# Kernel tuning notes

Measured on AMD Instinct MI355X. Metric: run time of the kernel, lower is better.

The kernel has to match this reference:

```python
import jax, jax.numpy as jnp
import numpy as np

jax.config.update("jax_enable_x64", True)

B, H, W = 16384, 19, 19
MAX_FLOOD = min(H * W // 4, 100)  # = 90, as in the torch module


def _count_neighbors(m):
    # m: [B,H,W] float. Sum of 4 orthogonal neighbors (zero-padded edges).
    up = jnp.pad(m[:, :-1, :], ((0, 0), (1, 0), (0, 0)))
    down = jnp.pad(m[:, 1:, :], ((0, 0), (0, 1), (0, 0)))
    left = jnp.pad(m[:, :, :-1], ((0, 0), (0, 0), (1, 0)))
    right = jnp.pad(m[:, :, 1:], ((0, 0), (0, 0), (0, 1)))
    return up + down + left + right


def _dilate(m):
    # m: [B,H,W] bool. OR of 4 orthogonal neighbors (False-padded edges).
    up = jnp.pad(m[:, :-1, :], ((0, 0), (1, 0), (0, 0)))
    down = jnp.pad(m[:, 1:, :], ((0, 0), (0, 1), (0, 0)))
    left = jnp.pad(m[:, :, :-1], ((0, 0), (0, 0), (1, 0)))
    right = jnp.pad(m[:, :, 1:], ((0, 0), (0, 0), (0, 1)))
    return up | down | left | right


def _flood_fill(seeds, mask):
    # Iterative neighbor expansion within mask, bounded iters + early exit.
    def cond(st):
        _, changed, i = st
        return changed & (i < MAX_FLOOD)

    def body(st):
        g, _, i = st
        exp = _dilate(g) & mask & ~g
        return (g | exp, exp.any(), i + 1)

    g, _, _ = jax.lax.while_loop(cond, body, (seeds, seeds.any(), jnp.int32(0)))
    return g


def setup_inputs() -> dict:
    key = jax.random.key(0)
    k1, k2, k3, k4, k5, k6 = jax.random.split(key, 6)
    # 0 = empty, 1 = black, 2 = white (planes never overlap)
    board = jax.random.randint(k1, (B, H, W), 0, 3)
    stones = jnp.stack([board == 1, board == 2], axis=1).astype(jnp.float32)
    current_player = jax.random.randint(k2, (B,), 0, 2).astype(jnp.int32)
    ko_rc = jax.random.randint(k3, (B, 2), 0, H).astype(jnp.int32)
    has_ko = jax.random.uniform(k4, (B,)) < 0.25
    ko_points = jnp.where(has_ko[:, None], ko_rc, jnp.int32(-1))
    hmax = np.iinfo(np.int64).max
    zobrist_stones = jax.random.randint(k5, (2, H, W), 0, hmax, dtype=jnp.int64)
    zobrist_turn = jax.random.randint(k6, (2,), 0, hmax, dtype=jnp.int64)
    position_hash = jnp.zeros((B,), jnp.int64)
    return {
        "stones": stones,
        "current_player": current_player,
        "ko_points": ko_points,
        "zobrist_stones": zobrist_stones,
        "zobrist_turn": zobrist_turn,
        "position_hash": position_hash,
    }


def reference(stones, current_player, ko_points, zobrist_stones, zobrist_turn, position_hash):
    stones_b = stones > 0.5                       # [B,2,H,W] bool
    empty_f = 1.0 - stones.sum(axis=1)            # [B,H,W] float (0/1)
    empty = ~stones_b.any(axis=1)                 # empty_mask
    liberties = _count_neighbors(empty_f)         # float liberty count per point

    # legal = empty points with at least one empty neighbor
    legal = empty & (liberties > 0.0)

    # capture moves: opponent stones with exactly one liberty
    cp = current_player.astype(jnp.int32)
    opp = jnp.take_along_axis(stones_b, (1 - cp)[:, None, None, None], axis=1)[:, 0]
    vulnerable = opp & (jnp.round(liberties).astype(jnp.int32) == 1)
    cap = empty & (_count_neighbors(vulnerable.astype(jnp.float32)) > 0.0)
    legal = legal | cap

    # ko restriction: mask the single ko point per game (if set)
    valid_ko = ko_points[:, 0] >= 0
    r_eq = jnp.arange(H)[None, :, None] == ko_points[:, 0][:, None, None]
    c_eq = jnp.arange(W)[None, None, :] == ko_points[:, 1][:, None, None]
    legal = legal & ~(valid_ko[:, None, None] & r_eq & c_eq)

    # flood fill the full groups-in-atari within opponent stones
    groups = _flood_fill(vulnerable, opp)

    # zobrist hash: XOR of stone hashes over the board + turn toggle
    contrib = jnp.where(stones_b, zobrist_stones[None], jnp.int64(0))  # [B,2,H,W]
    board_hash = jax.lax.reduce(contrib, np.int64(0), jax.lax.bitwise_xor, (1, 2, 3))
    new_hash = position_hash ^ board_hash ^ zobrist_turn[cp] ^ zobrist_turn[1 - cp]

    return (liberties, legal, groups, new_hash)
```

## Files before the change

kernel.cpp:

```cpp
#include <hip/hip_runtime.h>
#include <stdint.h>

#define WW 19
#define NP 361
#define M19 0x7FFFFu
#define BPB 32
#define TPB 512
#define BBSTR 25
#define PLSTR 97

__device__ __forceinline__ uint32_t rev19(uint32_t x) { return __brev(x) >> 13; }

__device__ __forceinline__ uint32_t runfill(uint32_t g, uint32_t m, uint32_t rm) {
  const uint32_t up = g | (m & ((m + g) ^ m ^ g));
  const uint32_t rg = rev19(g);
  const uint32_t dn = rg | (rm & ((rm + rg) ^ rm ^ rg));
  return up | rev19(dn);
}

__global__ __launch_bounds__(TPB, 4) void go_fused(
    const float* __restrict__ stones, const int* __restrict__ cur,
    const int* __restrict__ ko, const int* __restrict__ zob,
    const int* __restrict__ zturn, const int* __restrict__ phash,
    float* __restrict__ out, int B) {
  __shared__ uint32_t bbuf[BPB * BBSTR];
  __shared__ uint32_t pl[BPB * PLSTR];

  const int wid = threadIdx.x >> 6;
  const int lane = threadIdx.x & 63;
  const size_t NB = (size_t)B * NP;

  int zb[6], zw[6];
#pragma unroll
  for (int i = 0; i < 6; ++i) {
    const int p = i * 64 + lane;
    zb[i] = (p < NP) ? zob[p] : 0;
    zw[i] = (p < NP) ? zob[NP + p] : 0;
  }
  const int zt = zturn[0] ^ zturn[1];

#pragma unroll
  for (int k = 0; k < 4; ++k) {
    const int lb = wid * 4 + k;
    const int b = blockIdx.x * BPB + lb;
    if (b < B) {
      const float* sb = stones + (size_t)b * (2 * NP);
      int acc = 0;
#pragma unroll
      for (int i = 0; i < 6; ++i) {
        const int p = i * 64 + lane;
        const bool inb = p < NP;
        const float bv = inb ? sb[p] : 0.0f;
        const float wv = inb ? sb[NP + p] : 0.0f;
        const bool bs = bv > 0.5f, wsn = wv > 0.5f;
        const uint64_t bbm = __ballot(bs);
        const uint64_t wbm = __ballot(wsn);
        if (lane < 4) {
          const uint64_t src = (lane < 2) ? bbm : wbm;
          const uint32_t vv = (lane & 1) ? (uint32_t)(src >> 32) : (uint32_t)src;
          bbuf[lb * BBSTR + i * 4 + lane] = vv;
        }
        acc ^= zb[i] & (bs ? -1 : 0);
        acc ^= zw[i] & (wsn ? -1 : 0);
      }
#pragma unroll
      for (int off = 32; off > 0; off >>= 1) acc ^= __shfl_xor(acc, off, 64);
      if (lane == 0) out[3 * NB + b] = (float)(phash[b] ^ acc ^ zt);
    }
  }
  __syncthreads();

  if (threadIdx.x < BPB) {
    const int lb = threadIdx.x;
    const int b = blockIdx.x * BPB + lb;
    if (b < B) {
      uint64_t bmw[6], wmw[6];
#pragma unroll
      for (int i = 0; i < 6; ++i) {
        const uint32_t* q = &bbuf[lb * BBSTR + 4 * i];
        bmw[i] = (uint64_t)q[0] | ((uint64_t)q[1] << 32);
        wmw[i] = (uint64_t)q[2] | ((uint64_t)q[3] << 32);
      }
      const int cp = cur[b];
      uint32_t m[WW], e[WW];
#pragma unroll
      for (int r = 0; r < WW; ++r) {
        const int bit = WW * r;
        const int w = bit >> 6, sh = bit & 63;
        uint64_t xb = bmw[w] >> sh;
        uint64_t xw = wmw[w] >> sh;
        if (sh > 45) { xb |= bmw[w + 1] << (64 - sh); xw |= wmw[w + 1] << (64 - sh); }
        const uint32_t br = (uint32_t)xb & M19;
        const uint32_t wr = (uint32_t)xw & M19;
        m[r] = (cp == 0) ? wr : br;
        e[r] = ~(br | wr) & M19;
      }

      uint32_t* pb = &pl[lb * PLSTR];
      uint32_t vul[WW];
#pragma unroll
      for (int r = 0; r < WW; ++r) {
        const uint32_t u = (r > 0) ? e[r - 1] : 0u;
        const uint32_t d = (r < WW - 1) ? e[r + 1] : 0u;
        const uint32_t l = (e[r] << 1) & M19;
        const uint32_t rr = e[r] >> 1;
        const uint32_t s1 = u ^ d, c1 = u & d;
        const uint32_t s2 = l ^ rr, c2 = l & rr;
        const uint32_t cc = s1 & s2;
        const uint32_t L0 = s1 ^ s2;
        const uint32_t L1 = c1 ^ c2 ^ cc;
        pb[r] = L0;
        pb[19 + r] = L1;
        pb[38 + r] = (c1 & c2) | (cc & (c1 | c2));
        vul[r] = m[r] & L0 & ~L1;
      }

      const int2 kk = ((const int2*)ko)[b];
#pragma unroll
      for (int r = 0; r < WW; ++r) {
        const uint32_t u = (r > 0) ? e[r - 1] : 0u;
        const uint32_t d = (r < WW - 1) ? e[r + 1] : 0u;
        const uint32_t nbv = ((r > 0) ? vul[r - 1] : 0u) |
                             ((r < WW - 1) ? vul[r + 1] : 0u) |
                             ((vul[r] << 1) & M19) | (vul[r] >> 1);
        uint32_t leg = e[r] & (u | d | ((e[r] << 1) & M19) | (e[r] >> 1));
        leg |= e[r] & nbv;
        if (kk.x == r) leg &= ~(1u << kk.y);
        pb[57 + r] = leg;
      }

      uint32_t g[WW], rm[WW];
#pragma unroll
      for (int r = 0; r < WW; ++r) {
        rm[r] = rev19(m[r]);
        g[r] = runfill(vul[r], m[r], rm[r]);
      }
      for (int it = 0; it < 90; ++it) {
        uint32_t ex[WW], any = 0;
#pragma unroll
        for (int r = 0; r < WW; ++r) {
          const uint32_t nb = ((r > 0) ? g[r - 1] : 0u) |
                              ((r < WW - 1) ? g[r + 1] : 0u);
          ex[r] = nb & m[r] & ~g[r];
          any |= ex[r];
        }
        if (!__any(any != 0u)) break;
#pragma unroll
        for (int r = 0; r < WW; ++r) g[r] = runfill(g[r] | ex[r], m[r], rm[r]);
      }
#pragma unroll
      for (int r = 0; r < WW; ++r) pb[76 + r] = g[r];
    }
  }
  __syncthreads();

#pragma unroll
  for (int k = 0; k < 4; ++k) {
    const int lb = wid * 4 + k;
    const int b = blockIdx.x * BPB + lb;
    if (b < B) {
      float* o0 = out + (size_t)b * NP;
      const uint32_t* pb = &pl[lb * PLSTR];
#pragma unroll
      for (int i = 0; i < 6; ++i) {
        const int p = i * 64 + lane;
        if (p < NP) {
          const int r = (27 * p) >> 9;
          const int c = p - 19 * r;
          const uint32_t l0 = (pb[r] >> c) & 1u;
          const uint32_t l1 = (pb[19 + r] >> c) & 1u;
          const uint32_t l2 = (pb[38 + r] >> c) & 1u;
          o0[p] = (float)(l0 + 2u * l1 + 4u * l2);
          o0[NB + p] = (float)((pb[57 + r] >> c) & 1u);
          o0[2 * NB + p] = (float)((pb[76 + r] >> c) & 1u);
        }
      }
    }
  }
}

extern "C" void kernel_launch(void* const* d_in, const int* in_sizes, int n_in,
                              void* d_out, int out_size, void* d_ws,
                              size_t ws_size, hipStream_t stream) {
  const float* stones = (const float*)d_in[0];
  const int* cur = (const int*)d_in[1];
  const int* ko = (const int*)d_in[2];
  const int* zob = (const int*)d_in[3];
  const int* zturn = (const int*)d_in[4];
  const int* phash = (const int*)d_in[5];
  float* out = (float*)d_out;

  const int B = in_sizes[0] / (2 * NP);
  const int blocks = (B + BPB - 1) / BPB;
  go_fused<<<blocks, TPB, 0, stream>>>(stones, cur, ko, zob, zturn, phash, out,
                                       B);
}
```

Measured before the change: 33.48 us.

## Halve block size, use sweep-based flood fill, and vectorize output stores

Blocks shrink to 16 boards and 256 threads, raising the number of blocks and changing occupancy. The flood fill now does forward and backward row sweeps that carry growth across rows within each iteration, which should need fewer iterations; the cap drops to 45 sweep pairs. The zobrist XOR reductions for the four boards are batched into one interleaved shuffle loop. Full blocks write outputs as contiguous float4 stores over the block's flat range, which needs index division by 361 via a multiply trick and assumes 16-byte alignment.

```diff
diff --git a/kernel.cpp b/kernel.cpp
--- a/kernel.cpp
+++ b/kernel.cpp
@@ -4,21 +4,22 @@
 #define WW 19
 #define NP 361
 #define M19 0x7FFFFu
-#define BPB 32
-#define TPB 512
+#define BPB 16
+#define TPB 256
 #define BBSTR 25
 #define PLSTR 97
 
 __device__ __forceinline__ uint32_t rev19(uint32_t x) { return __brev(x) >> 13; }
 
-__device__ __forceinline__ uint32_t runfill(uint32_t g, uint32_t m, uint32_t rm) {
+__device__ __forceinline__ uint32_t runfill(uint32_t g, uint32_t m) {
   const uint32_t up = g | (m & ((m + g) ^ m ^ g));
+  const uint32_t rm = rev19(m);
   const uint32_t rg = rev19(g);
   const uint32_t dn = rg | (rm & ((rm + rg) ^ rm ^ rg));
   return up | rev19(dn);
 }
 
-__global__ __launch_bounds__(TPB, 4) void go_fused(
+__global__ __launch_bounds__(TPB, 2) void go_fused(
     const float* __restrict__ stones, const int* __restrict__ cur,
     const int* __restrict__ ko, const int* __restrict__ zob,
     const int* __restrict__ zturn, const int* __restrict__ phash,
@@ -28,6 +29,7 @@
 
   const int wid = threadIdx.x >> 6;
   const int lane = threadIdx.x & 63;
+  const int b0 = blockIdx.x * BPB;
   const size_t NB = (size_t)B * NP;
 
   int zb[6], zw[6];
@@ -39,13 +41,14 @@
   }
   const int zt = zturn[0] ^ zturn[1];
 
+  int acc[4];
 #pragma unroll
   for (int k = 0; k < 4; ++k) {
     const int lb = wid * 4 + k;
-    const int b = blockIdx.x * BPB + lb;
+    const int b = b0 + lb;
+    acc[k] = 0;
     if (b < B) {
       const float* sb = stones + (size_t)b * (2 * NP);
-      int acc = 0;
 #pragma unroll
       for (int i = 0; i < 6; ++i) {
         const int p = i * 64 + lane;
@@ -60,19 +63,28 @@
           const uint32_t vv = (lane & 1) ? (uint32_t)(src >> 32) : (uint32_t)src;
           bbuf[lb * BBSTR + i * 4 + lane] = vv;
         }
-        acc ^= zb[i] & (bs ? -1 : 0);
-        acc ^= zw[i] & (wsn ? -1 : 0);
-      }
-#pragma unroll
-      for (int off = 32; off > 0; off >>= 1) acc ^= __shfl_xor(acc, off, 64);
-      if (lane == 0) out[3 * NB + b] = (float)(phash[b] ^ acc ^ zt);
+        acc[k] ^= zb[i] & (bs ? -1 : 0);
+        acc[k] ^= zw[i] & (wsn ? -1 : 0);
+      }
+    }
+  }
+#pragma unroll
+  for (int off = 32; off > 0; off >>= 1) {
+#pragma unroll
+    for (int k = 0; k < 4; ++k) acc[k] ^= __shfl_xor(acc[k], off, 64);
+  }
+  if (lane == 0) {
+#pragma unroll
+    for (int k = 0; k < 4; ++k) {
+      const int b = b0 + wid * 4 + k;
+      if (b < B) out[3 * NB + b] = (float)(phash[b] ^ acc[k] ^ zt);
     }
   }
   __syncthreads();
 
   if (threadIdx.x < BPB) {
     const int lb = threadIdx.x;
-    const int b = blockIdx.x * BPB + lb;
+    const int b = b0 + lb;
     if (b < B) {
       uint64_t bmw[6], wmw[6];
 #pragma unroll
@@ -129,24 +141,29 @@
         pb[57 + r] = leg;
       }
 
-      uint32_t g[WW], rm[WW];
-#pragma unroll
-      for (int r = 0; r < WW; ++r) {
-        rm[r] = rev19(m[r]);
-        g[r] = runfill(vul[r], m[r], rm[r]);
-      }
-      for (int it = 0; it < 90; ++it) {
-        uint32_t ex[WW], any = 0;
+      uint32_t g[WW];
+#pragma unroll
+      for (int r = 0; r < WW; ++r) g[r] = runfill(vul[r], m[r]);
+      for (int it = 0; it < 45; ++it) {
+        uint32_t chg = 0, prev = 0;
 #pragma unroll
         for (int r = 0; r < WW; ++r) {
-          const uint32_t nb = ((r > 0) ? g[r - 1] : 0u) |
-                              ((r < WW - 1) ? g[r + 1] : 0u);
-          ex[r] = nb & m[r] & ~g[r];
-          any |= ex[r];
-        }
-        if (!__any(any != 0u)) break;
-#pragma unroll
-        for (int r = 0; r < WW; ++r) g[r] = runfill(g[r] | ex[r], m[r], rm[r]);
+          uint32_t t = g[r] | (prev & m[r]);
+          t = runfill(t, m[r]);
+          chg |= t ^ g[r];
+          g[r] = t;
+          prev = t;
+        }
+        prev = 0;
+#pragma unroll
+        for (int r = WW - 1; r >= 0; --r) {
+          uint32_t t = g[r] | (prev & m[r]);
+          t = runfill(t, m[r]);
+          chg |= t ^ g[r];
+          g[r] = t;
+          prev = t;
+        }
+        if (!__any(chg != 0u)) break;
       }
 #pragma unroll
       for (int r = 0; r < WW; ++r) pb[76 + r] = g[r];
@@ -154,25 +171,53 @@
   }
   __syncthreads();
 
-#pragma unroll
-  for (int k = 0; k < 4; ++k) {
-    const int lb = wid * 4 + k;
-    const int b = blockIdx.x * BPB + lb;
-    if (b < B) {
-      float* o0 = out + (size_t)b * NP;
-      const uint32_t* pb = &pl[lb * PLSTR];
-#pragma unroll
-      for (int i = 0; i < 6; ++i) {
-        const int p = i * 64 + lane;
-        if (p < NP) {
-          const int r = (27 * p) >> 9;
-          const int c = p - 19 * r;
-          const uint32_t l0 = (pb[r] >> c) & 1u;
-          const uint32_t l1 = (pb[19 + r] >> c) & 1u;
-          const uint32_t l2 = (pb[38 + r] >> c) & 1u;
-          o0[p] = (float)(l0 + 2u * l1 + 4u * l2);
-          o0[NB + p] = (float)((pb[57 + r] >> c) & 1u);
-          o0[2 * NB + p] = (float)((pb[76 + r] >> c) & 1u);
+  if (b0 + BPB <= B) {
+    float4* s0 = (float4*)(out + (size_t)b0 * NP);
+    float4* s1 = (float4*)(out + NB + (size_t)b0 * NP);
+    float4* s2 = (float4*)(out + 2 * NB + (size_t)b0 * NP);
+    const int nq = BPB * NP / 4;
+    for (int q = threadIdx.x; q < nq; q += TPB) {
+      float t0[4], t1[4], t2[4];
+#pragma unroll
+      for (int j = 0; j < 4; ++j) {
+        const int id = q * 4 + j;
+        const int lb = (id * 92949) >> 25;
+        const int p = id - lb * NP;
+        const int r = (p * 27) >> 9;
+        const int c = p - r * WW;
+        const uint32_t* pb = &pl[lb * PLSTR];
+        const uint32_t l0 = (pb[r] >> c) & 1u;
+        const uint32_t l1 = (pb[19 + r] >> c) & 1u;
+        const uint32_t l2 = (pb[38 + r] >> c) & 1u;
+        t0[j] = (float)(l0 + 2u * l1 + 4u * l2);
+        t1[j] = (float)((pb[57 + r] >> c) & 1u);
+        t2[j] = (float)((pb[76 + r] >> c) & 1u);
+      }
+      s0[q] = make_float4(t0[0], t0[1], t0[2], t0[3]);
+      s1[q] = make_float4(t1[0], t1[1], t1[2], t1[3]);
+      s2[q] = make_float4(t2[0], t2[1], t2[2], t2[3]);
+    }
+  } else {
+#pragma unroll
+    for (int k = 0; k < 4; ++k) {
+      const int lb = wid * 4 + k;
+      const int b = b0 + lb;
+      if (b < B) {
+        float* o0 = out + (size_t)b * NP;
+        const uint32_t* pb = &pl[lb * PLSTR];
+#pragma unroll
+        for (int i = 0; i < 6; ++i) {
+          const int p = i * 64 + lane;
+          if (p < NP) {
+            const int r = (p * 27) >> 9;
+            const int c = p - r * WW;
+            const uint32_t l0 = (pb[r] >> c) & 1u;
+            const uint32_t l1 = (pb[19 + r] >> c) & 1u;
+            const uint32_t l2 = (pb[38 + r] >> c) & 1u;
+            o0[p] = (float)(l0 + 2u * l1 + 4u * l2);
+            o0[NB + p] = (float)((pb[57 + r] >> c) & 1u);
+            o0[2 * NB + p] = (float)((pb[76 + r] >> c) & 1u);
+          }
         }
       }
     }
```

Measured after the change: 32.74 us. 1.02x faster.
